# Kernel optimization log

Hardware: AMD Instinct MI355X
Metric: run time of the kernel (lower is better)

## Reference

```python
import jax, jax.numpy as jnp
import numpy as np
from jax import lax

NUM_SEGMENTS = 50
HIDDEN = 128
IN_CH = 64
LOGSIG_DIM = IN_CH + IN_CH * (IN_CH - 1) // 2 + IN_CH  # level1 + Levy area + startpoint


def setup_inputs() -> dict:
    key = jax.random.key(0)
    k0, k1, k2, k3, k4 = jax.random.split(key, 5)
    B, C, T, V = 16, IN_CH, 200, 25
    x = jax.random.normal(k0, (B, C, T, V), dtype=jnp.float32)
    s = 1.0 / np.sqrt(HIDDEN).astype(np.float32)
    W_ih = jax.random.uniform(k1, (4 * HIDDEN, LOGSIG_DIM), jnp.float32, -s, s)
    W_hh = jax.random.uniform(k2, (4 * HIDDEN, HIDDEN), jnp.float32, -s, s)
    b_ih = jax.random.uniform(k3, (4 * HIDDEN,), jnp.float32, -s, s)
    b_hh = jax.random.uniform(k4, (4 * HIDDEN,), jnp.float32, -s, s)
    return {"x": x, "W_ih": W_ih, "W_hh": W_hh, "b_ih": b_ih, "b_hh": b_hh}


def _segment_logsig(xn):
    # xn: (N, C, T). Split T into NUM_SEGMENTS chunks; level-2 log-signature per chunk.
    N, C, T = xn.shape
    L = T // NUM_SEGMENTS  # points per segment
    p = xn.transpose(0, 2, 1).reshape(N, NUM_SEGMENTS, L, C)  # path points
    start = p[:, :, 0]                                  # (N,S,C) segment startpoint
    inc = p[:, :, 1:] - p[:, :, :-1]                    # (N,S,L-1,C) increments
    dev = p[:, :, :-1] - start[:, :, None]              # (N,S,L-1,C) p_t - p_0
    # Level-2 iterated integrals (cross terms): S2_ij = sum_t dev_t,i * inc_t,j
    S2 = jnp.einsum('nsti,nstj->nsij', dev, inc)        # (N,S,C,C)
    A = 0.5 * (S2 - S2.transpose(0, 1, 3, 2))           # Levy area (antisymmetric part)
    iu, ju = jnp.triu_indices(C, k=1)
    levy = A[:, :, iu, ju]                              # (N,S,C(C-1)/2)
    lvl1 = p[:, :, -1] - start                          # (N,S,C) level-1 term
    return jnp.concatenate([lvl1, levy, start], axis=-1)  # (N,S,LOGSIG_DIM)


def _lstm(seq, W_ih, W_hh, b_ih, b_hh):
    # seq: (N, S, F). Single-layer unidirectional LSTM, torch gate order (i,f,g,o).
    N = seq.shape[0]
    x_proj = jnp.einsum('nsf,gf->nsg', seq, W_ih) + b_ih + b_hh  # (N,S,4H)

    def step(carry, xt):
        h, c = carry
        gates = xt + h @ W_hh.T
        i, f, g, o = jnp.split(gates, 4, axis=-1)
        c = jax.nn.sigmoid(f) * c + jax.nn.sigmoid(i) * jnp.tanh(g)
        h = jax.nn.sigmoid(o) * jnp.tanh(c)
        return (h, c), h

    h0 = jnp.zeros((N, HIDDEN), seq.dtype)
    c0 = jnp.zeros((N, HIDDEN), seq.dtype)
    _, hs = lax.scan(step, (h0, c0), x_proj.transpose(1, 0, 2))
    return hs.transpose(1, 0, 2)  # (N,S,H)


def reference(x, W_ih, W_hh, b_ih, b_hh):
    B, C, T, V = x.shape
    xn = x.transpose(0, 3, 1, 2).reshape(B * V, C, T)
    ls = _segment_logsig(xn)                      # (B*V, S, LOGSIG_DIM)
    h = _lstm(ls, W_ih, W_hh, b_ih, b_hh)          # (B*V, S, H)
    out = h.reshape(B, V, NUM_SEGMENTS, HIDDEN).transpose(0, 3, 2, 1)
    return out  # (B, H, S, V)
```

## Files before the change

kernel.cpp:

```cpp
#include <hip/hip_runtime.h>
#include <stdint.h>

#define NSEG 50
#define HID 128
#define KDIM 2144
#define KD2 2176
#define KD2B 4352
#define NROW 20000
#define NROW_PAD 20096
#define GATES 512
#define NSEQ 400

typedef __attribute__((ext_vector_type(8))) _Float16 f16x8;
typedef __attribute__((ext_vector_type(4))) float f32x4;
typedef __attribute__((ext_vector_type(4))) uint32_t u32x4;

#define GLB_SPACE __attribute__((address_space(1)))
#define LDS_SPACE __attribute__((address_space(3)))

__device__ __forceinline__ void g2lds16(const void* g, void* l) {
    __builtin_amdgcn_global_load_lds((const GLB_SPACE uint32_t*)g,
                                     (LDS_SPACE uint32_t*)l, 16, 0, 0);
}

__global__ __launch_bounds__(256) void prep_kernel(const float* __restrict__ Wih,
                                                   const float* __restrict__ Whh,
                                                   const float* __restrict__ bih,
                                                   const float* __restrict__ bhh,
                                                   _Float16* __restrict__ wh,
                                                   _Float16* __restrict__ whh16,
                                                   float* __restrict__ bias) {
    int idx = blockIdx.x * 256 + threadIdx.x;
    const int nwih = 512 * KD2;
    const int nwhh = 512 * HID;
    if (idx < nwih) {
        int row = idx / KD2;
        int k = idx - row * KD2;
        wh[idx] = (k < KDIM) ? (_Float16)Wih[row * KDIM + k] : (_Float16)0.0f;
    } else if (idx < nwih + nwhh) {
        int q = idx - nwih;
        whh16[q] = (_Float16)Whh[q];
    } else if (idx < nwih + nwhh + 512) {
        int g = idx - nwih - nwhh;
        bias[g] = bih[g] + bhh[g];
    }
}

__global__ __launch_bounds__(256) void feat_kernel(const float* __restrict__ x,
                                                   _Float16* __restrict__ feat) {
    int bid = blockIdx.x;
    int b = bid / NSEG;
    int s = bid - b * NSEG;
    int tid = threadIdx.x;

    __shared__ float pbuf[64 * 100];
    __shared__ __align__(16) float4 uv4[25 * 64];

    for (int i = tid; i < 6400; i += 256) {
        int c = i / 100;
        int r = i - c * 100;
        pbuf[c * 100 + r] = x[(((size_t)b * 64 + c) * 200 + 4 * s) * 25 + r];
    }
    if (tid < 800) {
        int v = tid >> 5;
        int k = 2144 + (tid & 31);
        size_t m = ((size_t)(b * 25 + v)) * NSEG + s;
        feat[m * KD2 + k] = (_Float16)0.0f;
    }
    __syncthreads();

    for (int i = tid; i < 1600; i += 256) {
        int v = i >> 6;
        int c = i & 63;
        float p0 = pbuf[c * 100 + v];
        float p1 = pbuf[c * 100 + 25 + v];
        float p2 = pbuf[c * 100 + 50 + v];
        float p3 = pbuf[c * 100 + 75 + v];
        uv4[v * 64 + c] = make_float4(p1 - p0, p2 - p0, p2 - p1, p3 - p2);
        size_t m = ((size_t)(b * 25 + v)) * NSEG + s;
        feat[m * KD2 + c] = (_Float16)(p3 - p0);
        feat[m * KD2 + 2080 + c] = (_Float16)p0;
    }
    __syncthreads();

    for (int ch = 0; ch < 8; ch++) {
        int pidx = ch * 256 + tid;
        if (pidx < 2016) {
            float disc = 16129.0f - 8.0f * (float)pidx;
            int i = (int)((127.0f - sqrtf(disc)) * 0.5f);
            int off = 63 * i - (i * (i - 1)) / 2;
            while (off > pidx) { i--; off = 63 * i - (i * (i - 1)) / 2; }
            while (63 * (i + 1) - ((i + 1) * i) / 2 <= pidx) { i++; off = 63 * i - (i * (i - 1)) / 2; }
            int j = pidx - off + i + 1;
            int k = 64 + pidx;
            for (int v = 0; v < 25; v++) {
                float4 a = uv4[v * 64 + i];
                float4 bb = uv4[v * 64 + j];
                float val = 0.5f * (a.x * bb.z - bb.x * a.z + a.y * bb.w - bb.y * a.w);
                size_t m = ((size_t)(b * 25 + v)) * NSEG + s;
                feat[m * KD2 + k] = (_Float16)val;
            }
        }
    }
}

__global__ __launch_bounds__(256, 3) void gemm_kernel(const _Float16* __restrict__ feat,
                                                      const _Float16* __restrict__ wh,
                                                      const float* __restrict__ bias,
                                                      _Float16* __restrict__ xproj2) {
    int bid = blockIdx.x;
    int x = bid & 7;
    int t = bid >> 3;
    int nb = t & 3;
    int mt = (t >> 2) * 8 + x;
    if (mt >= 157) return;
    int m0 = mt * 128;
    int n0 = nb * 128;
    int tid = threadIdx.x;
    int wave = tid >> 6;
    int lane = tid & 63;
    int quad = lane >> 4;
    int l15 = lane & 15;
    int wm = (wave & 1) * 64;
    int wn = (wave >> 1) * 64;

    int r8 = lane >> 3;
    int gcol = ((lane & 7) * 16) ^ (r8 * 16);

    __shared__ __align__(16) _Float16 smem[16896];
    char* As = (char*)smem;
    char* Bs = (char*)smem + 128 * 128;

    const f32x4 z4 = {0.f, 0.f, 0.f, 0.f};
    f32x4 acc[4][4];
    for (int i = 0; i < 4; i++)
        for (int j = 0; j < 4; j++) acc[i][j] = z4;

    const char* featB = (const char*)feat;
    const char* whB = (const char*)wh;

    for (int kt = 0; kt < 34; kt++) {
        size_t kb = (size_t)kt * 128;
        __syncthreads();
        for (int it = 0; it < 4; it++) {
            int rb = it * 32 + wave * 8;
            g2lds16(featB + (size_t)(m0 + rb + r8) * KD2B + kb + gcol, As + rb * 128);
            g2lds16(whB + (size_t)(n0 + rb + r8) * KD2B + kb + gcol, Bs + rb * 128);
        }
        __syncthreads();

        for (int ks = 0; ks < 2; ks++) {
            int off = ((ks * 64) | (quad * 16)) ^ ((l15 & 7) * 16);
            f16x8 af[4], bf[4];
            for (int tt = 0; tt < 4; tt++) {
                af[tt] = *(const f16x8*)(As + (wm + tt * 16 + l15) * 128 + off);
                bf[tt] = *(const f16x8*)(Bs + (wn + tt * 16 + l15) * 128 + off);
            }
            for (int mtl = 0; mtl < 4; mtl++)
                for (int ntl = 0; ntl < 4; ntl++)
                    acc[mtl][ntl] = __builtin_amdgcn_mfma_f32_16x16x32_f16(af[mtl], bf[ntl], acc[mtl][ntl], 0, 0, 0);
        }
    }

    __syncthreads();
    for (int ntl = 0; ntl < 4; ntl++) {
        int nl = wn + ntl * 16 + l15;
        float bv = bias[n0 + nl];
        for (int mtl = 0; mtl < 4; mtl++)
            for (int r = 0; r < 4; r++) {
                int ml = wm + mtl * 16 + quad * 4 + r;
                smem[ml * 132 + nl] = (_Float16)(acc[mtl][ntl][r] + bv);
            }
    }
    __syncthreads();
    {
        int row = tid >> 1;
        int seg = tid & 1;
        int m = m0 + row;
        if (m < NROW) {
            unsigned q = (unsigned)m / 50u;
            unsigned s = (unsigned)m - q * 50u;
            const char* src = (const char*)smem + row * 264 + seg * 128;
            char* dst = (char*)xproj2 + ((size_t)s * NSEQ + q) * 1024 + (size_t)n0 * 2 + seg * 128;
            for (int i = 0; i < 8; i++)
                *(u32x4*)(dst + i * 16) = *(const u32x4*)(src + i * 16);
        }
    }
}

__global__ __launch_bounds__(512, 2) void lstm_kernel(const _Float16* __restrict__ xproj2,
                                                      const _Float16* __restrict__ whh,
                                                      _Float16* __restrict__ hseq) {
    int bid = blockIdx.x;
    int tid = threadIdx.x;
    int wave = tid >> 6;
    int lane = tid & 63;
    int quad = lane >> 4;
    int col = lane & 15;
    int hid = wave * 16 + col;

    __shared__ __align__(16) char xbuf[25 * 4 * 1040];
    __shared__ __align__(16) _Float16 hst[NSEG * 4 * HID];
    __shared__ __align__(16) _Float16 hbuf[2][4 * 144];

    f16x8 bfrag[4][4];
    for (int g = 0; g < 4; g++) {
        int n = g * 128 + hid;
        for (int kq = 0; kq < 4; kq++)
            bfrag[g][kq] = *(const f16x8*)(whh + (size_t)n * HID + kq * 32 + quad * 8);
    }
    for (int i = tid; i < 2 * 4 * 144; i += 512) ((_Float16*)hbuf)[i] = (_Float16)0.0f;
    float cst = 0.0f;

    const char* xsrc = (const char*)xproj2;
    for (int r = wave; r < 100; r += 8)
        g2lds16(xsrc + ((size_t)((r >> 2) * NSEQ + bid * 4 + (r & 3))) * 1024 + lane * 16,
                xbuf + r * 1040);
    __syncthreads();

    const f32x4 z4 = {0.f, 0.f, 0.f, 0.f};
    for (int half = 0; half < 2; half++) {
        for (int ss = 0; ss < 25; ss++) {
            int s = half * 25 + ss;
            int cur = s & 1;
            int nxt = cur ^ 1;

            f16x8 afrag[4];
            for (int kq = 0; kq < 4; kq++)
                afrag[kq] = *(const f16x8*)(&hbuf[cur][(col & 3) * 144 + kq * 32 + quad * 8]);

            float xp[4];
            for (int g = 0; g < 4; g++)
                xp[g] = (float)(*(const _Float16*)(xbuf + (ss * 4 + quad) * 1040 +
                               (g * 128 + hid) * 2));

            f32x4 acc[4];
            for (int g = 0; g < 4; g++) {
                acc[g] = z4;
                for (int kq = 0; kq < 4; kq++)
                    acc[g] = __builtin_amdgcn_mfma_f32_16x16x32_f16(afrag[kq], bfrag[g][kq], acc[g], 0, 0, 0);
            }

            float gv[4];
            for (int g = 0; g < 4; g++) {
                float lo = (quad & 1) ? acc[g][1] : acc[g][0];
                float hi = (quad & 1) ? acc[g][3] : acc[g][2];
                gv[g] = (quad & 2) ? hi : lo;
            }

            float ip = gv[0] + xp[0];
            float fp = gv[1] + xp[1];
            float gp = gv[2] + xp[2];
            float op = gv[3] + xp[3];
            float si = __fdividef(1.0f, 1.0f + __expf(-ip));
            float sf = __fdividef(1.0f, 1.0f + __expf(-fp));
            float so = __fdividef(1.0f, 1.0f + __expf(-op));
            float eg = __expf(-2.0f * gp);
            float tg = __fdividef(1.0f - eg, 1.0f + eg);
            cst = sf * cst + si * tg;
            float ec = __expf(-2.0f * cst);
            float tc = __fdividef(1.0f - ec, 1.0f + ec);
            float hv = so * tc;
            _Float16 hv16 = (_Float16)hv;
            hbuf[nxt][quad * 144 + hid] = hv16;
            hst[(s * 4 + quad) * 128 + hid] = hv16;
            __syncthreads();
        }
        if (half == 0) {
            for (int r = wave; r < 100; r += 8)
                g2lds16(xsrc + ((size_t)((25 + (r >> 2)) * NSEQ + bid * 4 + (r & 3))) * 1024 + lane * 16,
                        xbuf + r * 1040);
            __syncthreads();
        }
    }

    const u32x4* src = (const u32x4*)hst;
    for (int i = tid; i < 3200; i += 512) {
        int s = i >> 6;
        int rem = i & 63;
        int seq = rem >> 4;
        int seg = rem & 15;
        u32x4 v = src[i];
        *(u32x4*)((char*)hseq + ((size_t)(s * NSEQ + bid * 4 + seq)) * 256 + seg * 16) = v;
    }
}

__global__ __launch_bounds__(256) void tr_kernel(const _Float16* __restrict__ hseq,
                                                 float* __restrict__ out) {
    int bid = blockIdx.x;
    int b = bid / NSEG;
    int s = bid - b * NSEG;
    int tid = threadIdx.x;

    __shared__ _Float16 buf[25 * 130];

    const uint32_t* src32 = (const uint32_t*)(hseq + ((size_t)s * NSEQ + b * 25) * HID);
    uint32_t* buf32 = (uint32_t*)buf;
    for (int i = tid; i < 1600; i += 256) {
        int v = i >> 6;
        int d = i & 63;
        buf32[v * 65 + d] = src32[i];
    }
    __syncthreads();
    for (int i = tid; i < 3200; i += 256) {
        int hid = i / 25;
        int v = i - hid * 25;
        out[(((size_t)b * 128 + hid) * NSEG + s) * 25 + v] = (float)buf[v * 130 + hid];
    }
}

extern "C" void kernel_launch(void* const* d_in, const int* in_sizes, int n_in,
                              void* d_out, int out_size, void* d_ws, size_t ws_size,
                              hipStream_t stream) {
    const float* x = (const float*)d_in[0];
    const float* Wih = (const float*)d_in[1];
    const float* Whh = (const float*)d_in[2];
    const float* bih = (const float*)d_in[3];
    const float* bhh = (const float*)d_in[4];
    float* out = (float*)d_out;

    char* ws = (char*)d_ws;
    size_t off = 0;
    _Float16* feat = (_Float16*)(ws + off);   off += (size_t)NROW_PAD * KD2 * 2;
    _Float16* xproj2 = (_Float16*)(ws + off); off += (size_t)NSEG * NSEQ * GATES * 2;
    _Float16* hseq = (_Float16*)(ws + off);   off += (size_t)NSEG * NSEQ * HID * 2;
    _Float16* wh = (_Float16*)(ws + off);     off += (size_t)512 * KD2 * 2;
    _Float16* whh16 = (_Float16*)(ws + off);  off += (size_t)512 * HID * 2;
    float* bias = (float*)(ws + off);         off += 512 * 4;

    int prep_total = 512 * KD2 + 512 * HID + 512;
    hipLaunchKernelGGL(prep_kernel, dim3((prep_total + 255) / 256), dim3(256), 0, stream,
                       Wih, Whh, bih, bhh, wh, whh16, bias);
    hipLaunchKernelGGL(feat_kernel, dim3(16 * NSEG), dim3(256), 0, stream, x, feat);
    hipLaunchKernelGGL(gemm_kernel, dim3(640), dim3(256), 0, stream, feat, wh, bias, xproj2);
    hipLaunchKernelGGL(lstm_kernel, dim3(100), dim3(512), 0, stream, xproj2, whh16, hseq);
    hipLaunchKernelGGL(tr_kernel, dim3(16 * NSEG), dim3(256), 0, stream, hseq, out);
}
```

Measured before the change: 220.5 us.

## Fuse weight prep into feature kernel, tile Levy-area writes, double-buffer GEMM

Folds the weight conversion kernel into the feature kernel as extra blocks, removing one launch. The Levy-area features are reordered into 4x8 tiles so each thread writes vectorised f16x8 stores, and W_ih columns are permuted to match. The GEMM gains a double-buffered LDS stage so the next k-tile load overlaps the MFMAs. LDS use doubles, so occupancy drops from 3 to 2 blocks per CU, and the permutation tables add indexing complexity.

New measurement: 237.7 us. 1.08x slower.

```diff
diff --git a/kernel.cpp b/kernel.cpp
--- a/kernel.cpp
+++ b/kernel.cpp
@@ -12,6 +12,7 @@
 #define NSEQ 400
 
 typedef __attribute__((ext_vector_type(8))) _Float16 f16x8;
+typedef __attribute__((ext_vector_type(4))) _Float16 f16x4;
 typedef __attribute__((ext_vector_type(4))) float f32x4;
 typedef __attribute__((ext_vector_type(4))) uint32_t u32x4;
 
@@ -23,43 +24,97 @@
                                      (LDS_SPACE uint32_t*)l, 16, 0, 0);
 }
 
-__global__ __launch_bounds__(256) void prep_kernel(const float* __restrict__ Wih,
+__device__ const uint8_t TILES[56] = {
+    0x01,0x02,0x03,0x04,0x05,0x06,0x07,
+    0x09,0x0a,0x0b,0x0c,0x0d,0x0e,0x0f,
+    0x12,0x13,0x14,0x15,0x16,0x17,
+    0x1a,0x1b,0x1c,0x1d,0x1e,0x1f,
+    0x23,0x24,0x25,0x26,0x27,
+    0x2b,0x2c,0x2d,0x2e,0x2f,
+    0x34,0x35,0x36,0x37,
+    0x3c,0x3d,0x3e,0x3f,
+    0x45,0x46,0x47,
+    0x4d,0x4e,0x4f,
+    0x56,0x57,
+    0x5e,0x5f,
+    0x67,
+    0x6f,
+};
+__device__ const int8_t TRI_I[6] = {0,0,0,1,1,2};
+__device__ const int8_t TRI_J[6] = {1,2,3,2,3,3};
+
+__global__ __launch_bounds__(512) void feat_kernel(const float* __restrict__ x,
+                                                   const float* __restrict__ Wih,
                                                    const float* __restrict__ Whh,
                                                    const float* __restrict__ bih,
                                                    const float* __restrict__ bhh,
+                                                   _Float16* __restrict__ feat,
                                                    _Float16* __restrict__ wh,
                                                    _Float16* __restrict__ whh16,
                                                    float* __restrict__ bias) {
-    int idx = blockIdx.x * 256 + threadIdx.x;
-    const int nwih = 512 * KD2;
-    const int nwhh = 512 * HID;
-    if (idx < nwih) {
-        int row = idx / KD2;
-        int k = idx - row * KD2;
-        wh[idx] = (k < KDIM) ? (_Float16)Wih[row * KDIM + k] : (_Float16)0.0f;
-    } else if (idx < nwih + nwhh) {
-        int q = idx - nwih;
-        whh16[q] = (_Float16)Whh[q];
-    } else if (idx < nwih + nwhh + 512) {
-        int g = idx - nwih - nwhh;
-        bias[g] = bih[g] + bhh[g];
-    }
-}
-
-__global__ __launch_bounds__(256) void feat_kernel(const float* __restrict__ x,
-                                                   _Float16* __restrict__ feat) {
     int bid = blockIdx.x;
+    int tid = threadIdx.x;
+
+    if (bid >= 800) {
+        const int nwih = 512 * KD2;
+        const int nwhh = 512 * HID;
+        const int total = nwih + nwhh + 512;
+        for (int idx = (bid - 800) * 512 + tid; idx < total; idx += 64 * 512) {
+            if (idx < nwih) {
+                int g = idx / KD2;
+                int k = idx - g * KD2;
+                float wv = 0.0f;
+                if (k < KDIM) {
+                    int kold;
+                    if (k < 64 || k >= 2080) kold = k;
+                    else {
+                        int kl = k - 64;
+                        int i, j;
+                        if (kl < 1792) {
+                            int t = kl >> 5, r = kl & 31;
+                            int ab = TILES[t];
+                            i = ((ab >> 3) << 2) + (r >> 3);
+                            j = ((ab & 7) << 3) + (r & 7);
+                        } else if (kl < 1920) {
+                            int d = (kl - 1792) >> 4, r = (kl - 1792) & 15;
+                            int a = d << 1;
+                            i = (a << 2) + (r >> 2);
+                            j = (a << 2) + 4 + (r & 3);
+                        } else {
+                            int qq = kl - 1920;
+                            int a = qq / 6, e = qq - a * 6;
+                            i = (a << 2) + TRI_I[e];
+                            j = (a << 2) + TRI_J[e];
+                        }
+                        kold = 64 + 63 * i - (i * (i - 1)) / 2 + (j - i - 1);
+                    }
+                    wv = Wih[g * KDIM + kold];
+                }
+                wh[idx] = (_Float16)wv;
+            } else if (idx < nwih + nwhh) {
+                whh16[idx - nwih] = (_Float16)Whh[idx - nwih];
+            } else {
+                int g = idx - nwih - nwhh;
+                bias[g] = bih[g] + bhh[g];
+            }
+        }
+        return;
+    }
+
     int b = bid / NSEG;
     int s = bid - b * NSEG;
-    int tid = threadIdx.x;
-
-    __shared__ float pbuf[64 * 100];
-    __shared__ __align__(16) float4 uv4[25 * 64];
-
-    for (int i = tid; i < 6400; i += 256) {
-        int c = i / 100;
-        int r = i - c * 100;
-        pbuf[c * 100 + r] = x[(((size_t)b * 64 + c) * 200 + 4 * s) * 25 + r];
+
+    __shared__ __align__(16) float4 uv4T[1600];
+
+    for (int i = tid; i < 1600; i += 512) {
+        int c = i / 25;
+        int v = i - c * 25;
+        const float* xp = x + (((size_t)b * 64 + c) * 200 + 4 * s) * 25 + v;
+        float p0 = xp[0], p1 = xp[25], p2 = xp[50], p3 = xp[75];
+        uv4T[i] = make_float4(p1 - p0, p2 - p0, p2 - p1, p3 - p2);
+        size_t m = ((size_t)(b * 25 + v)) * NSEG + s;
+        feat[m * KD2 + c] = (_Float16)(p3 - p0);
+        feat[m * KD2 + 2080 + c] = (_Float16)p0;
     }
     if (tid < 800) {
         int v = tid >> 5;
@@ -69,42 +124,51 @@
     }
     __syncthreads();
 
-    for (int i = tid; i < 1600; i += 256) {
-        int v = i >> 6;
-        int c = i & 63;
-        float p0 = pbuf[c * 100 + v];
-        float p1 = pbuf[c * 100 + 25 + v];
-        float p2 = pbuf[c * 100 + 50 + v];
-        float p3 = pbuf[c * 100 + 75 + v];
-        uv4[v * 64 + c] = make_float4(p1 - p0, p2 - p0, p2 - p1, p3 - p2);
-        size_t m = ((size_t)(b * 25 + v)) * NSEG + s;
-        feat[m * KD2 + c] = (_Float16)(p3 - p0);
-        feat[m * KD2 + 2080 + c] = (_Float16)p0;
-    }
-    __syncthreads();
-
-    for (int ch = 0; ch < 8; ch++) {
-        int pidx = ch * 256 + tid;
-        if (pidx < 2016) {
-            float disc = 16129.0f - 8.0f * (float)pidx;
-            int i = (int)((127.0f - sqrtf(disc)) * 0.5f);
-            int off = 63 * i - (i * (i - 1)) / 2;
-            while (off > pidx) { i--; off = 63 * i - (i * (i - 1)) / 2; }
-            while (63 * (i + 1) - ((i + 1) * i) / 2 <= pidx) { i++; off = 63 * i - (i * (i - 1)) / 2; }
-            int j = pidx - off + i + 1;
-            int k = 64 + pidx;
-            for (int v = 0; v < 25; v++) {
-                float4 a = uv4[v * 64 + i];
-                float4 bb = uv4[v * 64 + j];
-                float val = 0.5f * (a.x * bb.z - bb.x * a.z + a.y * bb.w - bb.y * a.w);
-                size_t m = ((size_t)(b * 25 + v)) * NSEG + s;
-                feat[m * KD2 + k] = (_Float16)val;
-            }
-        }
-    }
-}
-
-__global__ __launch_bounds__(256, 3) void gemm_kernel(const _Float16* __restrict__ feat,
+    int hw = tid >> 5;
+    int v = tid & 31;
+    bool act = v < 25;
+    int vc = act ? v : 0;
+    char* frow = (char*)feat + (((size_t)(b * 25 + vc)) * NSEG + s) * (size_t)(KD2 * 2);
+
+    for (int tt = hw; tt < 56; tt += 16) {
+        int ab = TILES[tt];
+        int i0 = (ab >> 3) << 2, j0 = (ab & 7) << 3;
+        float4 ui[4], vj[8];
+        for (int q = 0; q < 4; q++) ui[q] = uv4T[(i0 + q) * 25 + vc];
+        for (int w = 0; w < 8; w++) vj[w] = uv4T[(j0 + w) * 25 + vc];
+        for (int q = 0; q < 4; q++) {
+            f16x8 out;
+            for (int w = 0; w < 8; w++)
+                out[w] = (_Float16)(0.5f * (ui[q].x * vj[w].z + ui[q].y * vj[w].w
+                                          - vj[w].x * ui[q].z - vj[w].y * ui[q].w));
+            if (act) *(f16x8*)(frow + 128 + (tt << 6) + (q << 4)) = out;
+        }
+    }
+    if (hw >= 8) {
+        int d = hw - 8, a = d << 1, i0 = a << 2, j0 = i0 + 4;
+        float4 ui[4], vj[4];
+        for (int q = 0; q < 4; q++) ui[q] = uv4T[(i0 + q) * 25 + vc];
+        for (int w = 0; w < 4; w++) vj[w] = uv4T[(j0 + w) * 25 + vc];
+        for (int q = 0; q < 4; q++) {
+            f16x4 out;
+            for (int w = 0; w < 4; w++)
+                out[w] = (_Float16)(0.5f * (ui[q].x * vj[w].z + ui[q].y * vj[w].w
+                                          - vj[w].x * ui[q].z - vj[w].y * ui[q].w));
+            if (act) *(f16x4*)(frow + 3712 + (d << 5) + (q << 3)) = out;
+        }
+    }
+    {
+        int i0 = hw << 2;
+        for (int e = 0; e < 6; e++) {
+            int i = i0 + TRI_I[e], j = i0 + TRI_J[e];
+            float4 A = uv4T[i * 25 + vc], B = uv4T[j * 25 + vc];
+            float val = 0.5f * (A.x * B.z + A.y * B.w - B.x * A.z - B.y * A.w);
+            if (act) *(_Float16*)(frow + 3968 + hw * 12 + e * 2) = (_Float16)val;
+        }
+    }
+}
+
+__global__ __launch_bounds__(256, 2) void gemm_kernel(const _Float16* __restrict__ feat,
                                                       const _Float16* __restrict__ wh,
                                                       const float* __restrict__ bias,
                                                       _Float16* __restrict__ xproj2) {
@@ -127,9 +191,7 @@
     int r8 = lane >> 3;
     int gcol = ((lane & 7) * 16) ^ (r8 * 16);
 
-    __shared__ __align__(16) _Float16 smem[16896];
-    char* As = (char*)smem;
-    char* Bs = (char*)smem + 128 * 128;
+    __shared__ __align__(16) _Float16 smem[32768];
 
     const f32x4 z4 = {0.f, 0.f, 0.f, 0.f};
     f32x4 acc[4][4];
@@ -139,28 +201,37 @@
     const char* featB = (const char*)feat;
     const char* whB = (const char*)wh;
 
+#define STAGE(kt, bsel) do {                                                         \
+        size_t kb_ = (size_t)(kt) * 128;                                             \
+        char* As_ = (char*)smem + (bsel) * 32768;                                    \
+        char* Bs_ = As_ + 16384;                                                     \
+        for (int it = 0; it < 4; it++) {                                             \
+            int rb = it * 32 + wave * 8;                                             \
+            g2lds16(featB + (size_t)(m0 + rb + r8) * KD2B + kb_ + gcol, As_ + rb * 128); \
+            g2lds16(whB + (size_t)(n0 + rb + r8) * KD2B + kb_ + gcol, Bs_ + rb * 128);  \
+        } } while (0)
+
+    STAGE(0, 0);
     for (int kt = 0; kt < 34; kt++) {
-        size_t kb = (size_t)kt * 128;
+        int cur = kt & 1;
         __syncthreads();
-        for (int it = 0; it < 4; it++) {
-            int rb = it * 32 + wave * 8;
-            g2lds16(featB + (size_t)(m0 + rb + r8) * KD2B + kb + gcol, As + rb * 128);
-            g2lds16(whB + (size_t)(n0 + rb + r8) * KD2B + kb + gcol, Bs + rb * 128);
-        }
-        __syncthreads();
-
+        const char* As = (const char*)smem + cur * 32768;
+        const char* Bs = As + 16384;
+        f16x8 af[2][4], bf[2][4];
         for (int ks = 0; ks < 2; ks++) {
             int off = ((ks * 64) | (quad * 16)) ^ ((l15 & 7) * 16);
-            f16x8 af[4], bf[4];
             for (int tt = 0; tt < 4; tt++) {
-                af[tt] = *(const f16x8*)(As + (wm + tt * 16 + l15) * 128 + off);
-                bf[tt] = *(const f16x8*)(Bs + (wn + tt * 16 + l15) * 128 + off);
+                af[ks][tt] = *(const f16x8*)(As + (wm + tt * 16 + l15) * 128 + off);
+                bf[ks][tt] = *(const f16x8*)(Bs + (wn + tt * 16 + l15) * 128 + off);
             }
+        }
+        if (kt + 1 < 34) STAGE(kt + 1, cur ^ 1);
+        for (int ks = 0; ks < 2; ks++)
             for (int mtl = 0; mtl < 4; mtl++)
                 for (int ntl = 0; ntl < 4; ntl++)
-                    acc[mtl][ntl] = __builtin_amdgcn_mfma_f32_16x16x32_f16(af[mtl], bf[ntl], acc[mtl][ntl], 0, 0, 0);
-        }
-    }
+                    acc[mtl][ntl] = __builtin_amdgcn_mfma_f32_16x16x32_f16(af[ks][mtl], bf[ks][ntl], acc[mtl][ntl], 0, 0, 0);
+    }
+#undef STAGE
 
     __syncthreads();
     for (int ntl = 0; ntl < 4; ntl++) {
@@ -328,10 +399,8 @@
     _Float16* whh16 = (_Float16*)(ws + off);  off += (size_t)512 * HID * 2;
     float* bias = (float*)(ws + off);         off += 512 * 4;
 
-    int prep_total = 512 * KD2 + 512 * HID + 512;
-    hipLaunchKernelGGL(prep_kernel, dim3((prep_total + 255) / 256), dim3(256), 0, stream,
-                       Wih, Whh, bih, bhh, wh, whh16, bias);
-    hipLaunchKernelGGL(feat_kernel, dim3(16 * NSEG), dim3(256), 0, stream, x, feat);
+    hipLaunchKernelGGL(feat_kernel, dim3(864), dim3(512), 0, stream,
+                       x, Wih, Whh, bih, bhh, feat, wh, whh16, bias);
     hipLaunchKernelGGL(gemm_kernel, dim3(640), dim3(256), 0, stream, feat, wh, bias, xproj2);
     hipLaunchKernelGGL(lstm_kernel, dim3(100), dim3(512), 0, stream, xproj2, whh16, hseq);
     hipLaunchKernelGGL(tr_kernel, dim3(16 * NSEG), dim3(256), 0, stream, hseq, out);
```
